# Kernel tuning notes

Hardware: AMD Instinct MI355X
Metric: run time of the kernel (lower is better)

Reference implementation:

```python
import jax, jax.numpy as jnp
import numpy as np
from functools import partial

U = 1200   # thought_size (GRU units)
E = 620    # word_size
V = 20000  # vocab_size
B = 128    # batch
T = 64     # seq_len
LN_EPS = 1e-3  # Keras LayerNormalization default epsilon


def layernorm(x, gamma, beta, eps=LN_EPS):
    m = jnp.mean(x, axis=-1, keepdims=True)
    v = jnp.mean(jnp.square(x - m), axis=-1, keepdims=True)
    return gamma * (x - m) * jax.lax.rsqrt(v + eps) + beta


def gru_ln_direction(emb, kernel, rkernel, bias, ln0_g, ln0_b, ln3_g, ln3_b):
    """Run the LayerNorm-GRU (impl=2, reset_after=True) over emb [B,T,E].
    Returns final hidden state [B,U]."""
    input_bias, recurrent_bias = bias[0], bias[1]
    # Time-parallel input projection: [B,T,3U]
    x_proj = jnp.einsum('bte,eu->btu', emb, kernel) + input_bias
    x_proj_t = jnp.transpose(x_proj, (1, 0, 2))  # [T,B,3U]

    def step(h, xt):
        h_ln = layernorm(h, ln0_g, ln0_b)                      # LN on previous state
        inner = h_ln @ rkernel + recurrent_bias                # [B,3U]
        z = jax.nn.sigmoid(xt[:, :U] + inner[:, :U])
        r = jax.nn.sigmoid(xt[:, U:2 * U] + inner[:, U:2 * U])
        rec_h = r * inner[:, 2 * U:]
        hh = jnp.tanh(layernorm(xt[:, 2 * U:] + rec_h, ln3_g, ln3_b))
        h_new = z * h_ln + (1.0 - z) * hh
        return h_new, None

    h0 = jnp.zeros((emb.shape[0], U), dtype=emb.dtype)
    h_final, _ = jax.lax.scan(step, h0, x_proj_t)
    return h_final


def setup_inputs() -> dict:
    key = jax.random.key(0)
    ks = jax.random.split(key, 8)
    s = 0.05
    return {
        'sentences': jax.random.randint(ks[0], (B, T), 0, V),
        'embed': jax.random.normal(ks[1], (V, E), jnp.float32) * s,
        'fw_kernel': jax.random.normal(ks[2], (E, 3 * U), jnp.float32) * s,
        'fw_rkernel': jax.random.normal(ks[3], (U, 3 * U), jnp.float32) * s,
        'fw_bias': jax.random.normal(ks[4], (2, 3 * U), jnp.float32) * s,
        'fw_ln0_g': jnp.ones((U,), jnp.float32),
        'fw_ln0_b': jnp.zeros((U,), jnp.float32),
        'fw_ln3_g': jnp.ones((U,), jnp.float32),
        'fw_ln3_b': jnp.zeros((U,), jnp.float32),
        'bw_kernel': jax.random.normal(ks[5], (E, 3 * U), jnp.float32) * s,
        'bw_rkernel': jax.random.normal(ks[6], (U, 3 * U), jnp.float32) * s,
        'bw_bias': jax.random.normal(ks[7], (2, 3 * U), jnp.float32) * s,
        'bw_ln0_g': jnp.ones((U,), jnp.float32),
        'bw_ln0_b': jnp.zeros((U,), jnp.float32),
        'bw_ln3_g': jnp.ones((U,), jnp.float32),
        'bw_ln3_b': jnp.zeros((U,), jnp.float32),
    }


def reference(sentences, embed, fw_kernel, fw_rkernel, fw_bias,
              fw_ln0_g, fw_ln0_b, fw_ln3_g, fw_ln3_b,
              bw_kernel, bw_rkernel, bw_bias,
              bw_ln0_g, bw_ln0_b, bw_ln3_g, bw_ln3_b):
    embedding = jnp.tanh(embed[sentences])  # [B,T,E]
    forward_h = gru_ln_direction(embedding, fw_kernel, fw_rkernel, fw_bias,
                                 fw_ln0_g, fw_ln0_b, fw_ln3_g, fw_ln3_b)
    backward_h = gru_ln_direction(embedding[:, ::-1, :], bw_kernel, bw_rkernel, bw_bias,
                                  bw_ln0_g, bw_ln0_b, bw_ln3_g, bw_ln3_b)
    thought_vector = jnp.concatenate([forward_h, backward_h], axis=1)  # [B,2U]
    return thought_vector, embedding
```

## Files before the change

kernel.cpp:

```cpp
#include <hip/hip_runtime.h>
#include <hip/hip_bf16.h>

#define U_    1200
#define E_    620
#define B_    128
#define T_    64
#define N3    3600
#define NP    3712
#define KE    640
#define KU    1216
#define WIN   16
#define LN_EPS 1e-3f

#define GBLK  464
#define UBLK  128
#define TBLK  (GBLK + UBLK)

typedef __attribute__((ext_vector_type(8))) short short8;
typedef __attribute__((ext_vector_type(4))) float f32x4;
typedef _Float16 f16;
typedef __attribute__((ext_vector_type(8))) _Float16 half8;

constexpr size_t OFF_EMBH  = 0;
constexpr size_t SZ_EMB    = (size_t)8192 * KE * 2;
constexpr size_t OFF_EMBL  = OFF_EMBH + SZ_EMB;
constexpr size_t OFF_KTH   = OFF_EMBL + SZ_EMB;
constexpr size_t SZ_KT     = (size_t)2 * NP * KE * 2;
constexpr size_t OFF_KTL   = OFF_KTH + SZ_KT;
constexpr size_t OFF_RKF   = OFF_KTL + SZ_KT;
constexpr size_t SZ_RKF    = (size_t)2 * NP * KU * 2;
constexpr size_t OFF_XPW   = OFF_RKF + SZ_RKF;
constexpr size_t SZ_XPW    = (size_t)2 * WIN * B_ * NP * 4;
constexpr size_t OFF_INNER = OFF_XPW + SZ_XPW;
constexpr size_t SZ_INNER  = (size_t)8 * B_ * NP * 4;
constexpr size_t OFF_HLN   = OFF_INNER + SZ_INNER;
constexpr size_t SZ_HLN    = (size_t)2 * B_ * U_ * 4;
constexpr size_t OFF_HLFH  = OFF_HLN + SZ_HLN;
constexpr size_t SZ_HLF    = (size_t)2 * B_ * KU * 2;
constexpr size_t OFF_HLFL  = OFF_HLFH + SZ_HLF;

__device__ inline void lds_load16(const void* g, void* l) {
  __builtin_amdgcn_global_load_lds(
      (const __attribute__((address_space(1))) unsigned int*)g,
      (__attribute__((address_space(3))) unsigned int*)l, 16, 0, 0);
}

__device__ inline float sigmf(float x) { return 1.f / (1.f + expf(-x)); }

__device__ inline int swz_scol(int tid) {
  return (((tid & 7) ^ ((tid >> 3) & 7)) << 3);
}
__device__ inline int swz_off(int row, int kk, int lane) {
  return row * 64 + ((kk * 32 + ((lane >> 4) << 3)) ^ ((row & 7) << 3));
}

__global__ __launch_bounds__(256)
void embed_kernel(const int* __restrict__ sent, const float* __restrict__ embed,
                  float* __restrict__ out_emb,
                  __hip_bfloat16* __restrict__ embH, __hip_bfloat16* __restrict__ embL) {
  const int row = blockIdx.x;
  const int idx = sent[row];
  const float* src = embed + (size_t)idx * E_;
  for (int e = threadIdx.x; e < KE; e += 256) {
    float v = 0.f;
    if (e < E_) {
      v = tanhf(src[e]);
      out_emb[(size_t)row * E_ + e] = v;
    }
    const __hip_bfloat16 hi = __float2bfloat16(v);
    embH[(size_t)row * KE + e] = hi;
    embL[(size_t)row * KE + e] = __float2bfloat16(v - __bfloat162float(hi));
  }
}

__global__ __launch_bounds__(256)
void transpose_cast(const float* __restrict__ W0, const float* __restrict__ W1,
                    __hip_bfloat16* __restrict__ WtHi, __hip_bfloat16* __restrict__ WtLo,
                    int Kreal, int Kp) {
  const int d = blockIdx.z;
  const float* W = d ? W1 : W0;
  __hip_bfloat16* dstH = WtHi + (size_t)d * NP * Kp;
  __hip_bfloat16* dstL = WtLo + (size_t)d * NP * Kp;
  __shared__ float tile[32][33];
  const int n0 = blockIdx.x * 32, k0 = blockIdx.y * 32;
  const int tx = threadIdx.x, ty = threadIdx.y;
#pragma unroll
  for (int i = 0; i < 32; i += 8) {
    const int k = k0 + ty + i, n = n0 + tx;
    tile[ty + i][tx] = (k < Kreal && n < N3) ? W[(size_t)k * N3 + n] : 0.f;
  }
  __syncthreads();
#pragma unroll
  for (int i = 0; i < 32; i += 8) {
    const int n = n0 + ty + i, k = k0 + tx;
    const float v = tile[tx][ty + i];
    const __hip_bfloat16 hi = __float2bfloat16(v);
    dstH[(size_t)n * Kp + k] = hi;
    dstL[(size_t)n * Kp + k] = __float2bfloat16(v - __bfloat162float(hi));
  }
}

__global__ __launch_bounds__(256)
void transpose_cast_f16(const float* __restrict__ W0, const float* __restrict__ W1,
                        f16* __restrict__ Wt, int Kreal, int Kp) {
  const int d = blockIdx.z;
  const float* W = d ? W1 : W0;
  f16* dst = Wt + (size_t)d * NP * Kp;
  __shared__ float tile[32][33];
  const int n0 = blockIdx.x * 32, k0 = blockIdx.y * 32;
  const int tx = threadIdx.x, ty = threadIdx.y;
#pragma unroll
  for (int i = 0; i < 32; i += 8) {
    const int k = k0 + ty + i, n = n0 + tx;
    tile[ty + i][tx] = (k < Kreal && n < N3) ? W[(size_t)k * N3 + n] : 0.f;
  }
  __syncthreads();
#pragma unroll
  for (int i = 0; i < 32; i += 8) {
    const int n = n0 + ty + i, k = k0 + tx;
    dst[(size_t)n * Kp + k] = (f16)tile[tx][ty + i];
  }
}

__global__ __launch_bounds__(256)
void init_hln(const float* __restrict__ fw_b0, const float* __restrict__ bw_b0,
              float* __restrict__ hln, f16* __restrict__ hlfH, f16* __restrict__ hlfL) {
  const int idx = blockIdx.x * 256 + threadIdx.x;
  if (idx >= 2 * B_ * KU) return;
  const int k = idx % KU;
  const int rowd = idx / KU;
  const int d = rowd >> 7;
  float v = 0.f;
  if (k < U_) {
    v = (d ? bw_b0 : fw_b0)[k];
    hln[(size_t)rowd * U_ + k] = v;
  }
  const f16 hi = (f16)v;
  hlfH[idx] = hi;
  hlfL[idx] = (f16)(v - (float)hi);
}

__global__ __launch_bounds__(256)
void xwin_gemm(const __hip_bfloat16* __restrict__ embH, const __hip_bfloat16* __restrict__ embL,
               const __hip_bfloat16* __restrict__ kTH, const __hip_bfloat16* __restrict__ kTL,
               const float* __restrict__ fw_bias, const float* __restrict__ bw_bias,
               float* __restrict__ xpw, int w0) {
  constexpr int BM = 128, BN = 128, BK = 64;
  constexpr int WM = 64, WN = 64, FM = 4, FN = 4;
  constexpr int TA = BM * BK, TB = BN * BK;
  const int bid = blockIdx.x;
  const int w = (bid & 7) * 116 + (bid >> 3);
  const int d = w / 464;
  const int q = w % 464;
  const int nt = q / 16, mt = q % 16;
  const int m0 = mt * BM;
  const int n0 = nt * BN;

  const __hip_bfloat16* BH = kTH + (size_t)d * NP * KE;
  const __hip_bfloat16* BL = kTL + (size_t)d * NP * KE;

  const int tid = threadIdx.x;
  const int lane = tid & 63;
  const int wid = tid >> 6;
  const int wr = wid >> 1, wc = wid & 1;

  __shared__ __align__(16) __hip_bfloat16 As[2 * TA];
  __shared__ __align__(16) __hip_bfloat16 Bs[2 * TB];

  f32x4 acc[FM][FN] = {};

  const int srow = tid >> 3;
  const int scol = swz_scol(tid);

  for (int ks = 0; ks < KE / BK; ++ks) {
    const int k0 = ks * BK;
    __syncthreads();
#pragma unroll
    for (int it = 0; it < TA / 2048; ++it) {
      const int row = m0 + it * 32 + srow;
      const int b = row & 127, srel = row >> 7;
      const int txi = d ? (T_ - 1 - (w0 + srel)) : (w0 + srel);
      const size_t goff = (size_t)(b * T_ + txi) * KE + k0 + scol;
      lds_load16(embH + goff, As + it * 2048 + tid * 8);
      lds_load16(embL + goff, As + TA + it * 2048 + tid * 8);
    }
#pragma unroll
    for (int it = 0; it < TB / 2048; ++it) {
      const size_t goff = (size_t)(n0 + it * 32 + srow) * KE + k0 + scol;
      lds_load16(BH + goff, Bs + it * 2048 + tid * 8);
      lds_load16(BL + goff, Bs + TB + it * 2048 + tid * 8);
    }
    __syncthreads();
#pragma unroll
    for (int kk = 0; kk < BK / 32; ++kk) {
      short8 ah[FM], al[FM], bh[FN], bl[FN];
#pragma unroll
      for (int mi = 0; mi < FM; ++mi) {
        const int row = wr * WM + mi * 16 + (lane & 15);
        const int off = swz_off(row, kk, lane);
        ah[mi] = *(const short8*)(As + off);
        al[mi] = *(const short8*)(As + TA + off);
      }
#pragma unroll
      for (int ni = 0; ni < FN; ++ni) {
        const int row = wc * WN + ni * 16 + (lane & 15);
        const int off = swz_off(row, kk, lane);
        bh[ni] = *(const short8*)(Bs + off);
        bl[ni] = *(const short8*)(Bs + TB + off);
      }
#pragma unroll
      for (int mi = 0; mi < FM; ++mi)
#pragma unroll
        for (int ni = 0; ni < FN; ++ni) {
          acc[mi][ni] = __builtin_amdgcn_mfma_f32_16x16x32_bf16(ah[mi], bh[ni], acc[mi][ni], 0, 0, 0);
          acc[mi][ni] = __builtin_amdgcn_mfma_f32_16x16x32_bf16(ah[mi], bl[ni], acc[mi][ni], 0, 0, 0);
          acc[mi][ni] = __builtin_amdgcn_mfma_f32_16x16x32_bf16(al[mi], bh[ni], acc[mi][ni], 0, 0, 0);
        }
    }
  }

  const float* ib = d ? bw_bias : fw_bias;
#pragma unroll
  for (int mi = 0; mi < FM; ++mi)
#pragma unroll
    for (int ni = 0; ni < FN; ++ni) {
      const int gc = n0 + wc * WN + ni * 16 + (lane & 15);
      const float bv = (gc < N3) ? ib[gc] : 0.f;
      const int gr0 = m0 + wr * WM + mi * 16 + ((lane >> 4) << 2);
#pragma unroll
      for (int j = 0; j < 4; ++j) {
        const int gr = gr0 + j;
        const int b = gr & 127, srel = gr >> 7;
        const size_t off = ((size_t)(d * WIN + srel) * B_ + b) * NP + gc;
        xpw[off] = acc[mi][ni][j] + bv;
      }
    }
}

__device__ inline void breduce2(float& a, float& b, float* red, int tid) {
#pragma unroll
  for (int off = 32; off; off >>= 1) {
    a += __shfl_down(a, off, 64);
    b += __shfl_down(b, off, 64);
  }
  const int w = tid >> 6;
  __syncthreads();
  if ((tid & 63) == 0) { red[w] = a; red[4 + w] = b; }
  __syncthreads();
  a = red[0] + red[1] + red[2] + red[3];
  b = red[4] + red[5] + red[6] + red[7];
}

__global__ __launch_bounds__(256)
void step_fused(const f16* __restrict__ rkF,
                f16* __restrict__ hlfH, f16* __restrict__ hlfL,
                float* __restrict__ hln, float* __restrict__ inner,
                const float* __restrict__ xpw,
                const float* __restrict__ fw_bias, const float* __restrict__ bw_bias,
                const float* __restrict__ fw_ln0g, const float* __restrict__ fw_ln0b,
                const float* __restrict__ fw_ln3g, const float* __restrict__ fw_ln3b,
                const float* __restrict__ bw_ln0g, const float* __restrict__ bw_ln0b,
                const float* __restrict__ bw_ln3g, const float* __restrict__ bw_ln3b,
                float* __restrict__ out_tv,
                int dG, int doG, int dU, int tU, int doU) {
  __shared__ __align__(16) f16 smem[24576];
  __shared__ float red[8];

  const int bid = blockIdx.x;
  const int tid = threadIdx.x;

  if (bid < GBLK) {
    if (!doG) return;
    const int x  = bid & 7;
    const int kp = x >> 1;
    const int m  = x & 1;
    const int nt = bid >> 3;
    const int ks0 = kp * 5;
    const int ks1 = (kp == 3) ? 19 : (ks0 + 5);
    const int m0 = m * 64;
    const int n0 = nt * 64;

    const int lane = tid & 63;
    const int wid = tid >> 6;
    const int wr = wid >> 1, wc = wid & 1;

    const f16* WF = rkF + (size_t)dG * NP * KU;

    f32x4 acc[2][2] = {};
    const int srow = tid >> 3;
    const int scol = swz_scol(tid);

#define STG(buf_, ks_)                                                         \
  {                                                                            \
    const int k0s = (ks_) * 64;                                                \
    f16* base = smem + (buf_) * 12288;                                         \
    _Pragma("unroll")                                                          \
    for (int it = 0; it < 2; ++it) {                                           \
      const size_t ga = (size_t)(dG * B_ + m0 + it * 32 + srow) * KU + k0s + scol; \
      lds_load16(hlfH + ga, base + it * 2048 + tid * 8);                       \
      lds_load16(hlfL + ga, base + 4096 + it * 2048 + tid * 8);                \
      const size_t gb = (size_t)(n0 + it * 32 + srow) * KU + k0s + scol;       \
      lds_load16(WF + gb, base + 8192 + it * 2048 + tid * 8);                  \
    }                                                                          \
  }

    STG(0, ks0)
    __syncthreads();
    int cur = 0;
    for (int ks = ks0; ks < ks1; ++ks) {
      if (ks + 1 < ks1) STG(cur ^ 1, ks + 1)
      const f16* AH = smem + cur * 12288;
      const f16* AL = AH + 4096;
      const f16* BW = AH + 8192;
#pragma unroll
      for (int kk = 0; kk < 2; ++kk) {
        half8 ah[2], al[2], bv[2];
#pragma unroll
        for (int mi = 0; mi < 2; ++mi) {
          const int row = wr * 32 + mi * 16 + (lane & 15);
          const int off = swz_off(row, kk, lane);
          ah[mi] = *(const half8*)(AH + off);
          al[mi] = *(const half8*)(AL + off);
        }
#pragma unroll
        for (int nf = 0; nf < 2; ++nf) {
          const int row = wc * 32 + nf * 16 + (lane & 15);
          const int off = swz_off(row, kk, lane);
          bv[nf] = *(const half8*)(BW + off);
        }
#pragma unroll
        for (int mi = 0; mi < 2; ++mi)
#pragma unroll
          for (int nf = 0; nf < 2; ++nf) {
            acc[mi][nf] = __builtin_amdgcn_mfma_f32_16x16x32_f16(ah[mi], bv[nf], acc[mi][nf], 0, 0, 0);
            acc[mi][nf] = __builtin_amdgcn_mfma_f32_16x16x32_f16(al[mi], bv[nf], acc[mi][nf], 0, 0, 0);
          }
      }
      __syncthreads();
      cur ^= 1;
    }
#undef STG

    float* C = inner + (size_t)(dG * 4 + kp) * B_ * NP;
#pragma unroll
    for (int mi = 0; mi < 2; ++mi)
#pragma unroll
      for (int nf = 0; nf < 2; ++nf) {
        const int gc = n0 + wc * 32 + nf * 16 + (lane & 15);
        const int gr = m0 + wr * 32 + mi * 16 + ((lane >> 4) << 2);
#pragma unroll
        for (int j = 0; j < 4; ++j)
          C[(size_t)(gr + j) * NP + gc] = acc[mi][nf][j];
      }
    return;
  }

  if (!doU) return;
  const int r = bid - GBLK;
  const int d = dU;
  const int srel = tU & (WIN - 1);

  const float* rec0 = inner + ((size_t)(d * 4 + 0) * B_ + r) * NP;
  const float* rec1 = inner + ((size_t)(d * 4 + 1) * B_ + r) * NP;
  const float* rec2 = inner + ((size_t)(d * 4 + 2) * B_ + r) * NP;
  const float* rec3 = inner + ((size_t)(d * 4 + 3) * B_ + r) * NP;
  const float* xr = xpw + ((size_t)(d * WIN + srel) * B_ + r) * NP;
  const float* rb = (d ? bw_bias : fw_bias) + N3;
  const float* g0 = d ? bw_ln0g : fw_ln0g;
  const float* b0 = d ? bw_ln0b : fw_ln0b;
  const float* g3 = d ? bw_ln3g : fw_ln3g;
  const float* b3 = d ? bw_ln3b : fw_ln3b;
  float* hl = hln + ((size_t)d * B_ + r) * U_;
  f16* hlbH = hlfH + ((size_t)d * B_ + r) * KU;
  f16* hlbL = hlfL + ((size_t)d * B_ + r) * KU;

  float zv[5], cv[5], hv[5];
  float s1 = 0.f, s2 = 0.f;
#pragma unroll
  for (int i = 0; i < 5; ++i) {
    const int c = tid + i * 256;
    if (c < U_) {
      const float rz = (rec0[c] + rec1[c]) + (rec2[c] + rec3[c]);
      const float rg = (rec0[U_ + c] + rec1[U_ + c]) + (rec2[U_ + c] + rec3[U_ + c]);
      const float rh = (rec0[2 * U_ + c] + rec1[2 * U_ + c]) + (rec2[2 * U_ + c] + rec3[2 * U_ + c]);
      const float z  = sigmf(xr[c] + rz + rb[c]);
      const float rr = sigmf(xr[U_ + c] + rg + rb[U_ + c]);
      const float cand = xr[2 * U_ + c] + rr * (rh + rb[2 * U_ + c]);
      zv[i] = z; cv[i] = cand;
      s1 += cand; s2 += cand * cand;
    }
  }
  breduce2(s1, s2, red, tid);
  const float m1 = s1 / U_;
  const float is1 = rsqrtf(s2 / U_ - m1 * m1 + LN_EPS);

  float t1 = 0.f, t2 = 0.f;
#pragma unroll
  for (int i = 0; i < 5; ++i) {
    const int c = tid + i * 256;
    if (c < U_) {
      const float hh = tanhf(g3[c] * (cv[i] - m1) * is1 + b3[c]);
      const float hn = zv[i] * hl[c] + (1.f - zv[i]) * hh;
      hv[i] = hn;
      t1 += hn; t2 += hn * hn;
    }
  }
  breduce2(t1, t2, red, tid);
  const float m2 = t1 / U_;
  const float is2 = rsqrtf(t2 / U_ - m2 * m2 + LN_EPS);

#pragma unroll
  for (int i = 0; i < 5; ++i) {
    const int c = tid + i * 256;
    if (c < U_) {
      const float hlnew = g0[c] * (hv[i] - m2) * is2 + b0[c];
      hl[c] = hlnew;
      const f16 hi = (f16)hlnew;
      hlbH[c] = hi;
      hlbL[c] = (f16)(hlnew - (float)hi);
      if (tU == T_ - 1) out_tv[(size_t)r * 2400 + (size_t)d * U_ + c] = hv[i];
    }
  }
}

extern "C" void kernel_launch(void* const* d_in, const int* in_sizes, int n_in,
                              void* d_out, int out_size, void* d_ws, size_t ws_size,
                              hipStream_t stream) {
  const int*   sent      = (const int*)  d_in[0];
  const float* embed     = (const float*)d_in[1];
  const float* fw_kernel = (const float*)d_in[2];
  const float* fw_rkern  = (const float*)d_in[3];
  const float* fw_bias   = (const float*)d_in[4];
  const float* fw_ln0g   = (const float*)d_in[5];
  const float* fw_ln0b   = (const float*)d_in[6];
  const float* fw_ln3g   = (const float*)d_in[7];
  const float* fw_ln3b   = (const float*)d_in[8];
  const float* bw_kernel = (const float*)d_in[9];
  const float* bw_rkern  = (const float*)d_in[10];
  const float* bw_bias   = (const float*)d_in[11];
  const float* bw_ln0g   = (const float*)d_in[12];
  const float* bw_ln0b   = (const float*)d_in[13];
  const float* bw_ln3g   = (const float*)d_in[14];
  const float* bw_ln3b   = (const float*)d_in[15];

  uint8_t* ws = (uint8_t*)d_ws;
  __hip_bfloat16* embH  = (__hip_bfloat16*)(ws + OFF_EMBH);
  __hip_bfloat16* embL  = (__hip_bfloat16*)(ws + OFF_EMBL);
  __hip_bfloat16* kTH   = (__hip_bfloat16*)(ws + OFF_KTH);
  __hip_bfloat16* kTL   = (__hip_bfloat16*)(ws + OFF_KTL);
  f16*            rkF   = (f16*)(ws + OFF_RKF);
  float*          xpw   = (float*)(ws + OFF_XPW);
  float*          inner = (float*)(ws + OFF_INNER);
  float*          hln   = (float*)(ws + OFF_HLN);
  f16*            hlfH  = (f16*)(ws + OFF_HLFH);
  f16*            hlfL  = (f16*)(ws + OFF_HLFL);

  float* out_tv  = (float*)d_out;
  float* out_emb = (float*)d_out + (size_t)B_ * 2 * U_;

  embed_kernel<<<B_ * T_, 256, 0, stream>>>(sent, embed, out_emb, embH, embL);

  transpose_cast<<<dim3(NP / 32, KE / 32, 2), dim3(32, 8), 0, stream>>>(
      fw_kernel, bw_kernel, kTH, kTL, E_, KE);
  transpose_cast_f16<<<dim3(NP / 32, KU / 32, 2), dim3(32, 8), 0, stream>>>(
      fw_rkern, bw_rkern, rkF, U_, KU);

  init_hln<<<(2 * B_ * KU + 255) / 256, 256, 0, stream>>>(fw_ln0b, bw_ln0b,
                                                          hln, hlfH, hlfL);

#define SF(dG_, doG_, dU_, tU_, doU_)                                          \
  step_fused<<<TBLK, 256, 0, stream>>>(                                        \
      rkF, hlfH, hlfL, hln, inner, xpw,                                        \
      fw_bias, bw_bias, fw_ln0g, fw_ln0b, fw_ln3g, fw_ln3b,                    \
      bw_ln0g, bw_ln0b, bw_ln3g, bw_ln3b, out_tv,                              \
      dG_, doG_, dU_, tU_, doU_)

  for (int t = 0; t < T_; ++t) {
    SF(0, 1, 1, t - 1, (t > 0) ? 1 : 0);
    if ((t & (WIN - 1)) == 0)
      xwin_gemm<<<928, 256, 0, stream>>>(
          embH, embL, kTH, kTL, fw_bias, bw_bias, xpw, t);
    SF(1, 1, 0, t, 1);
  }
  SF(0, 0, 1, T_ - 1, 1);
#undef SF
}
```

Baseline: 1.788 ms.

## Fuse GRU step GEMM and update into one launch with flag-based sync

Before, each timestep ran as two staggered launches that interleaved one direction's GEMM with the other direction's update. Now one launch per timestep runs both directions' recurrent GEMM blocks and 256 update blocks. Update blocks spin on atomic counters in global memory until all GEMM blocks for their direction have stored their partial results. This halves the number of launches and removes the cross-direction stagger. The risk is a deadlock or stall if update blocks occupy CUs before the GEMM blocks get scheduled, plus the cost of relaxed atomic loads and stores on the partial results.

```diff
diff --git a/kernel.cpp b/kernel.cpp
--- a/kernel.cpp
+++ b/kernel.cpp
@@ -13,8 +13,7 @@
 #define LN_EPS 1e-3f
 
 #define GBLK  464
-#define UBLK  128
-#define TBLK  (GBLK + UBLK)
+#define TBLK  (2 * GBLK + 256)
 
 typedef __attribute__((ext_vector_type(8))) short short8;
 typedef __attribute__((ext_vector_type(4))) float f32x4;
@@ -38,6 +37,7 @@
 constexpr size_t OFF_HLFH  = OFF_HLN + SZ_HLN;
 constexpr size_t SZ_HLF    = (size_t)2 * B_ * KU * 2;
 constexpr size_t OFF_HLFL  = OFF_HLFH + SZ_HLF;
+constexpr size_t OFF_FLAGS = OFF_HLFL + SZ_HLF;
 
 __device__ inline void lds_load16(const void* g, void* l) {
   __builtin_amdgcn_global_load_lds(
@@ -46,6 +46,13 @@
 }
 
 __device__ inline float sigmf(float x) { return 1.f / (1.f + expf(-x)); }
+
+__device__ inline void astore(float* p, float v) {
+  __hip_atomic_store(p, v, __ATOMIC_RELAXED, __HIP_MEMORY_SCOPE_AGENT);
+}
+__device__ inline float aload(const float* p) {
+  return __hip_atomic_load(p, __ATOMIC_RELAXED, __HIP_MEMORY_SCOPE_AGENT);
+}
 
 __device__ inline int swz_scol(int tid) {
   return (((tid & 7) ^ ((tid >> 3) & 7)) << 3);
@@ -252,29 +259,29 @@
 }
 
 __global__ __launch_bounds__(256)
-void step_fused(const f16* __restrict__ rkF,
-                f16* __restrict__ hlfH, f16* __restrict__ hlfL,
-                float* __restrict__ hln, float* __restrict__ inner,
-                const float* __restrict__ xpw,
-                const float* __restrict__ fw_bias, const float* __restrict__ bw_bias,
-                const float* __restrict__ fw_ln0g, const float* __restrict__ fw_ln0b,
-                const float* __restrict__ fw_ln3g, const float* __restrict__ fw_ln3b,
-                const float* __restrict__ bw_ln0g, const float* __restrict__ bw_ln0b,
-                const float* __restrict__ bw_ln3g, const float* __restrict__ bw_ln3b,
-                float* __restrict__ out_tv,
-                int dG, int doG, int dU, int tU, int doU) {
+void step_all(const f16* __restrict__ rkF,
+              f16* __restrict__ hlfH, f16* __restrict__ hlfL,
+              float* __restrict__ hln, float* __restrict__ inner,
+              const float* __restrict__ xpw, int* __restrict__ flags,
+              const float* __restrict__ fw_bias, const float* __restrict__ bw_bias,
+              const float* __restrict__ fw_ln0g, const float* __restrict__ fw_ln0b,
+              const float* __restrict__ fw_ln3g, const float* __restrict__ fw_ln3b,
+              const float* __restrict__ bw_ln0g, const float* __restrict__ bw_ln0b,
+              const float* __restrict__ bw_ln3g, const float* __restrict__ bw_ln3b,
+              float* __restrict__ out_tv, int t) {
   __shared__ __align__(16) f16 smem[24576];
   __shared__ float red[8];
 
   const int bid = blockIdx.x;
   const int tid = threadIdx.x;
 
-  if (bid < GBLK) {
-    if (!doG) return;
-    const int x  = bid & 7;
+  if (bid < 2 * GBLK) {
+    const int dG = bid >= GBLK;
+    const int b2 = bid - dG * GBLK;
+    const int x  = b2 & 7;
     const int kp = x >> 1;
     const int m  = x & 1;
-    const int nt = bid >> 3;
+    const int nt = b2 >> 3;
     const int ks0 = kp * 5;
     const int ks1 = (kp == 3) ? 19 : (ks0 + 5);
     const int m0 = m * 64;
@@ -350,15 +357,26 @@
         const int gr = m0 + wr * 32 + mi * 16 + ((lane >> 4) << 2);
 #pragma unroll
         for (int j = 0; j < 4; ++j)
-          C[(size_t)(gr + j) * NP + gc] = acc[mi][nf][j];
+          astore(&C[(size_t)(gr + j) * NP + gc], acc[mi][nf][j]);
       }
+    __syncthreads();
+    if (tid == 0)
+      __hip_atomic_fetch_add(&flags[2 * t + dG], 1, __ATOMIC_RELAXED,
+                             __HIP_MEMORY_SCOPE_AGENT);
     return;
   }
 
-  if (!doU) return;
-  const int r = bid - GBLK;
-  const int d = dU;
-  const int srel = tU & (WIN - 1);
+  const int u = bid - 2 * GBLK;
+  const int d = u >> 7;
+  const int r = u & 127;
+  const int srel = t & (WIN - 1);
+
+  if (tid == 0) {
+    while (__hip_atomic_load(&flags[2 * t + d], __ATOMIC_RELAXED,
+                             __HIP_MEMORY_SCOPE_AGENT) < GBLK)
+      __builtin_amdgcn_s_sleep(8);
+  }
+  __syncthreads();
 
   const float* rec0 = inner + ((size_t)(d * 4 + 0) * B_ + r) * NP;
   const float* rec1 = inner + ((size_t)(d * 4 + 1) * B_ + r) * NP;
@@ -380,9 +398,12 @@
   for (int i = 0; i < 5; ++i) {
     const int c = tid + i * 256;
     if (c < U_) {
-      const float rz = (rec0[c] + rec1[c]) + (rec2[c] + rec3[c]);
-      const float rg = (rec0[U_ + c] + rec1[U_ + c]) + (rec2[U_ + c] + rec3[U_ + c]);
-      const float rh = (rec0[2 * U_ + c] + rec1[2 * U_ + c]) + (rec2[2 * U_ + c] + rec3[2 * U_ + c]);
+      const float rz = (aload(&rec0[c]) + aload(&rec1[c])) +
+                       (aload(&rec2[c]) + aload(&rec3[c]));
+      const float rg = (aload(&rec0[U_ + c]) + aload(&rec1[U_ + c])) +
+                       (aload(&rec2[U_ + c]) + aload(&rec3[U_ + c]));
+      const float rh = (aload(&rec0[2 * U_ + c]) + aload(&rec1[2 * U_ + c])) +
+                       (aload(&rec2[2 * U_ + c]) + aload(&rec3[2 * U_ + c]));
       const float z  = sigmf(xr[c] + rz + rb[c]);
       const float rr = sigmf(xr[U_ + c] + rg + rb[U_ + c]);
       const float cand = xr[2 * U_ + c] + rr * (rh + rb[2 * U_ + c]);
@@ -418,7 +439,7 @@
       const f16 hi = (f16)hlnew;
       hlbH[c] = hi;
       hlbL[c] = (f16)(hlnew - (float)hi);
-      if (tU == T_ - 1) out_tv[(size_t)r * 2400 + (size_t)d * U_ + c] = hv[i];
+      if (t == T_ - 1) out_tv[(size_t)r * 2400 + (size_t)d * U_ + c] = hv[i];
     }
   }
 }
@@ -454,9 +475,12 @@
   float*          hln   = (float*)(ws + OFF_HLN);
   f16*            hlfH  = (f16*)(ws + OFF_HLFH);
   f16*            hlfL  = (f16*)(ws + OFF_HLFL);
+  int*            flags = (int*)(ws + OFF_FLAGS);
 
   float* out_tv  = (float*)d_out;
   float* out_emb = (float*)d_out + (size_t)B_ * 2 * U_;
+
+  hipMemsetAsync(flags, 0, 2 * T_ * sizeof(int), stream);
 
   embed_kernel<<<B_ * T_, 256, 0, stream>>>(sent, embed, out_emb, embH, embL);
 
@@ -468,20 +492,13 @@
   init_hln<<<(2 * B_ * KU + 255) / 256, 256, 0, stream>>>(fw_ln0b, bw_ln0b,
                                                           hln, hlfH, hlfL);
 
-#define SF(dG_, doG_, dU_, tU_, doU_)                                          \
-  step_fused<<<TBLK, 256, 0, stream>>>(                                        \
-      rkF, hlfH, hlfL, hln, inner, xpw,                                        \
-      fw_bias, bw_bias, fw_ln0g, fw_ln0b, fw_ln3g, fw_ln3b,                    \
-      bw_ln0g, bw_ln0b, bw_ln3g, bw_ln3b, out_tv,                              \
-      dG_, doG_, dU_, tU_, doU_)
-
   for (int t = 0; t < T_; ++t) {
-    SF(0, 1, 1, t - 1, (t > 0) ? 1 : 0);
     if ((t & (WIN - 1)) == 0)
       xwin_gemm<<<928, 256, 0, stream>>>(
           embH, embL, kTH, kTL, fw_bias, bw_bias, xpw, t);
-    SF(1, 1, 0, t, 1);
-  }
-  SF(0, 0, 1, T_ - 1, 1);
-#undef SF
-}
+    step_all<<<TBLK, 256, 0, stream>>>(
+        rkF, hlfH, hlfL, hln, inner, xpw, flags,
+        fw_bias, bw_bias, fw_ln0g, fw_ln0b, fw_ln3g, fw_ln3b,
+        bw_ln0g, bw_ln0b, bw_ln3g, bw_ln3b, out_tv, t);
+  }
+}
```

Measured after the change: 3.123 ms. 1.75x slower.

## Fuse both GRU directions into one launch per step with in-kernel flag sync

Applied to the files above, without the earlier changes.

Each timestep previously took two launches, each pairing one direction's recurrent GEMM with the other direction's gate update. Now a single launch per step runs the gate-update blocks for both directions alongside GEMM blocks for both directions. The GEMM blocks spin on per-step atomic counters until all 128 update rows of their direction have written the new hidden state. Split-K drops from 4 to 2, the inner partials become parity double-buffered, and the LDS double buffering in the GEMM loop is removed. This roughly halves launch count and per-launch sync overhead. In exchange it depends on update blocks being scheduled before the spinning GEMM blocks, relies on relaxed atomics without explicit fences for visibility, and loses load/compute overlap in the GEMM.

```diff
diff --git a/kernel.cpp b/kernel.cpp
--- a/kernel.cpp
+++ b/kernel.cpp
@@ -12,9 +12,9 @@
 #define WIN   16
 #define LN_EPS 1e-3f
 
+#define UBLK  256
 #define GBLK  464
-#define UBLK  128
-#define TBLK  (GBLK + UBLK)
+#define TBLK  (UBLK + GBLK)
 
 typedef __attribute__((ext_vector_type(8))) short short8;
 typedef __attribute__((ext_vector_type(4))) float f32x4;
@@ -38,6 +38,7 @@
 constexpr size_t OFF_HLFH  = OFF_HLN + SZ_HLN;
 constexpr size_t SZ_HLF    = (size_t)2 * B_ * KU * 2;
 constexpr size_t OFF_HLFL  = OFF_HLFH + SZ_HLF;
+constexpr size_t OFF_FLAGS = OFF_HLFL + SZ_HLF;
 
 __device__ inline void lds_load16(const void* g, void* l) {
   __builtin_amdgcn_global_load_lds(
@@ -46,6 +47,10 @@
 }
 
 __device__ inline float sigmf(float x) { return 1.f / (1.f + expf(-x)); }
+
+__device__ inline void astore_u16(unsigned short* p, unsigned short v) {
+  __hip_atomic_store(p, v, __ATOMIC_RELAXED, __HIP_MEMORY_SCOPE_AGENT);
+}
 
 __device__ inline int swz_scol(int tid) {
   return (((tid & 7) ^ ((tid >> 3) & 7)) << 3);
@@ -252,33 +257,44 @@
 }
 
 __global__ __launch_bounds__(256)
-void step_fused(const f16* __restrict__ rkF,
-                f16* __restrict__ hlfH, f16* __restrict__ hlfL,
-                float* __restrict__ hln, float* __restrict__ inner,
-                const float* __restrict__ xpw,
-                const float* __restrict__ fw_bias, const float* __restrict__ bw_bias,
-                const float* __restrict__ fw_ln0g, const float* __restrict__ fw_ln0b,
-                const float* __restrict__ fw_ln3g, const float* __restrict__ fw_ln3b,
-                const float* __restrict__ bw_ln0g, const float* __restrict__ bw_ln0b,
-                const float* __restrict__ bw_ln3g, const float* __restrict__ bw_ln3b,
-                float* __restrict__ out_tv,
-                int dG, int doG, int dU, int tU, int doU) {
-  __shared__ __align__(16) f16 smem[24576];
+void step_one(const f16* __restrict__ rkF,
+              f16* __restrict__ hlfH, f16* __restrict__ hlfL,
+              float* __restrict__ hln, float* __restrict__ inner,
+              const float* __restrict__ xpw, int* __restrict__ flags,
+              const float* __restrict__ fw_bias, const float* __restrict__ bw_bias,
+              const float* __restrict__ fw_ln0g, const float* __restrict__ fw_ln0b,
+              const float* __restrict__ fw_ln3g, const float* __restrict__ fw_ln3b,
+              const float* __restrict__ bw_ln0g, const float* __restrict__ bw_ln0b,
+              const float* __restrict__ bw_ln3g, const float* __restrict__ bw_ln3b,
+              float* __restrict__ out_tv, int t, int doU, int doG) {
+  __shared__ __align__(16) f16 smem[12288];
   __shared__ float red[8];
 
   const int bid = blockIdx.x;
   const int tid = threadIdx.x;
 
-  if (bid < GBLK) {
+  if (bid >= UBLK) {
     if (!doG) return;
-    const int x  = bid & 7;
+    const int bid2 = bid - UBLK;
+    const int dG = bid2 >= 232;
+    const int b2 = bid2 - dG * 232;
+    const int x  = b2 & 3;
     const int kp = x >> 1;
     const int m  = x & 1;
-    const int nt = bid >> 3;
-    const int ks0 = kp * 5;
-    const int ks1 = (kp == 3) ? 19 : (ks0 + 5);
+    const int nt = b2 >> 2;
+    const int ks0 = kp ? 10 : 0;
+    const int ks1 = kp ? 19 : 10;
     const int m0 = m * 64;
     const int n0 = nt * 64;
+
+    if (doU) {
+      if (tid == 0) {
+        while (__hip_atomic_load(&flags[2 * t + dG], __ATOMIC_RELAXED,
+                                 __HIP_MEMORY_SCOPE_AGENT) < B_)
+          __builtin_amdgcn_s_sleep(2);
+      }
+      __syncthreads();
+    }
 
     const int lane = tid & 63;
     const int wid = tid >> 6;
@@ -290,28 +306,18 @@
     const int srow = tid >> 3;
     const int scol = swz_scol(tid);
 
-#define STG(buf_, ks_)                                                         \
-  {                                                                            \
-    const int k0s = (ks_) * 64;                                                \
-    f16* base = smem + (buf_) * 12288;                                         \
-    _Pragma("unroll")                                                          \
-    for (int it = 0; it < 2; ++it) {                                           \
-      const size_t ga = (size_t)(dG * B_ + m0 + it * 32 + srow) * KU + k0s + scol; \
-      lds_load16(hlfH + ga, base + it * 2048 + tid * 8);                       \
-      lds_load16(hlfL + ga, base + 4096 + it * 2048 + tid * 8);                \
-      const size_t gb = (size_t)(n0 + it * 32 + srow) * KU + k0s + scol;       \
-      lds_load16(WF + gb, base + 8192 + it * 2048 + tid * 8);                  \
-    }                                                                          \
-  }
-
-    STG(0, ks0)
-    __syncthreads();
-    int cur = 0;
     for (int ks = ks0; ks < ks1; ++ks) {
-      if (ks + 1 < ks1) STG(cur ^ 1, ks + 1)
-      const f16* AH = smem + cur * 12288;
-      const f16* AL = AH + 4096;
-      const f16* BW = AH + 8192;
+      const int k0s = ks * 64;
+      __syncthreads();
+#pragma unroll
+      for (int it = 0; it < 2; ++it) {
+        const size_t ga = (size_t)(dG * B_ + m0 + it * 32 + srow) * KU + k0s + scol;
+        lds_load16(hlfH + ga, smem + it * 2048 + tid * 8);
+        lds_load16(hlfL + ga, smem + 4096 + it * 2048 + tid * 8);
+        const size_t gb = (size_t)(n0 + it * 32 + srow) * KU + k0s + scol;
+        lds_load16(WF + gb, smem + 8192 + it * 2048 + tid * 8);
+      }
+      __syncthreads();
 #pragma unroll
       for (int kk = 0; kk < 2; ++kk) {
         half8 ah[2], al[2], bv[2];
@@ -319,14 +325,14 @@
         for (int mi = 0; mi < 2; ++mi) {
           const int row = wr * 32 + mi * 16 + (lane & 15);
           const int off = swz_off(row, kk, lane);
-          ah[mi] = *(const half8*)(AH + off);
-          al[mi] = *(const half8*)(AL + off);
+          ah[mi] = *(const half8*)(smem + off);
+          al[mi] = *(const half8*)(smem + 4096 + off);
         }
 #pragma unroll
         for (int nf = 0; nf < 2; ++nf) {
           const int row = wc * 32 + nf * 16 + (lane & 15);
           const int off = swz_off(row, kk, lane);
-          bv[nf] = *(const half8*)(BW + off);
+          bv[nf] = *(const half8*)(smem + 8192 + off);
         }
 #pragma unroll
         for (int mi = 0; mi < 2; ++mi)
@@ -336,12 +342,9 @@
             acc[mi][nf] = __builtin_amdgcn_mfma_f32_16x16x32_f16(al[mi], bv[nf], acc[mi][nf], 0, 0, 0);
           }
       }
-      __syncthreads();
-      cur ^= 1;
-    }
-#undef STG
-
-    float* C = inner + (size_t)(dG * 4 + kp) * B_ * NP;
+    }
+
+    float* C = inner + (size_t)((t & 1) * 4 + dG * 2 + kp) * B_ * NP;
 #pragma unroll
     for (int mi = 0; mi < 2; ++mi)
 #pragma unroll
@@ -356,14 +359,13 @@
   }
 
   if (!doU) return;
-  const int r = bid - GBLK;
-  const int d = dU;
+  const int tU = t - 1;
+  const int d = bid >> 7;
+  const int r = bid & 127;
   const int srel = tU & (WIN - 1);
 
-  const float* rec0 = inner + ((size_t)(d * 4 + 0) * B_ + r) * NP;
-  const float* rec1 = inner + ((size_t)(d * 4 + 1) * B_ + r) * NP;
-  const float* rec2 = inner + ((size_t)(d * 4 + 2) * B_ + r) * NP;
-  const float* rec3 = inner + ((size_t)(d * 4 + 3) * B_ + r) * NP;
+  const float* rec0 = inner + ((size_t)((tU & 1) * 4 + d * 2 + 0) * B_ + r) * NP;
+  const float* rec1 = inner + ((size_t)((tU & 1) * 4 + d * 2 + 1) * B_ + r) * NP;
   const float* xr = xpw + ((size_t)(d * WIN + srel) * B_ + r) * NP;
   const float* rb = (d ? bw_bias : fw_bias) + N3;
   const float* g0 = d ? bw_ln0g : fw_ln0g;
@@ -380,9 +382,9 @@
   for (int i = 0; i < 5; ++i) {
     const int c = tid + i * 256;
     if (c < U_) {
-      const float rz = (rec0[c] + rec1[c]) + (rec2[c] + rec3[c]);
-      const float rg = (rec0[U_ + c] + rec1[U_ + c]) + (rec2[U_ + c] + rec3[U_ + c]);
-      const float rh = (rec0[2 * U_ + c] + rec1[2 * U_ + c]) + (rec2[2 * U_ + c] + rec3[2 * U_ + c]);
+      const float rz = rec0[c] + rec1[c];
+      const float rg = rec0[U_ + c] + rec1[U_ + c];
+      const float rh = rec0[2 * U_ + c] + rec1[2 * U_ + c];
       const float z  = sigmf(xr[c] + rz + rb[c]);
       const float rr = sigmf(xr[U_ + c] + rg + rb[U_ + c]);
       const float cand = xr[2 * U_ + c] + rr * (rh + rb[2 * U_ + c]);
@@ -416,11 +418,16 @@
       const float hlnew = g0[c] * (hv[i] - m2) * is2 + b0[c];
       hl[c] = hlnew;
       const f16 hi = (f16)hlnew;
-      hlbH[c] = hi;
-      hlbL[c] = (f16)(hlnew - (float)hi);
+      const f16 lo = (f16)(hlnew - (float)hi);
+      astore_u16((unsigned short*)&hlbH[c], __builtin_bit_cast(unsigned short, hi));
+      astore_u16((unsigned short*)&hlbL[c], __builtin_bit_cast(unsigned short, lo));
       if (tU == T_ - 1) out_tv[(size_t)r * 2400 + (size_t)d * U_ + c] = hv[i];
     }
   }
+  __syncthreads();
+  if (tid == 0)
+    __hip_atomic_fetch_add(&flags[2 * t + d], 1, __ATOMIC_RELAXED,
+                           __HIP_MEMORY_SCOPE_AGENT);
 }
 
 extern "C" void kernel_launch(void* const* d_in, const int* in_sizes, int n_in,
@@ -454,9 +461,12 @@
   float*          hln   = (float*)(ws + OFF_HLN);
   f16*            hlfH  = (f16*)(ws + OFF_HLFH);
   f16*            hlfL  = (f16*)(ws + OFF_HLFL);
+  int*            flags = (int*)(ws + OFF_FLAGS);
 
   float* out_tv  = (float*)d_out;
   float* out_emb = (float*)d_out + (size_t)B_ * 2 * U_;
+
+  hipMemsetAsync(flags, 0, 2 * (T_ + 1) * sizeof(int), stream);
 
   embed_kernel<<<B_ * T_, 256, 0, stream>>>(sent, embed, out_emb, embH, embL);
 
@@ -468,20 +478,18 @@
   init_hln<<<(2 * B_ * KU + 255) / 256, 256, 0, stream>>>(fw_ln0b, bw_ln0b,
                                                           hln, hlfH, hlfL);
 
-#define SF(dG_, doG_, dU_, tU_, doU_)                                          \
-  step_fused<<<TBLK, 256, 0, stream>>>(                                        \
-      rkF, hlfH, hlfL, hln, inner, xpw,                                        \
+#define SO(t_, doU_, doG_)                                                     \
+  step_one<<<TBLK, 256, 0, stream>>>(                                          \
+      rkF, hlfH, hlfL, hln, inner, xpw, flags,                                 \
       fw_bias, bw_bias, fw_ln0g, fw_ln0b, fw_ln3g, fw_ln3b,                    \
-      bw_ln0g, bw_ln0b, bw_ln3g, bw_ln3b, out_tv,                              \
-      dG_, doG_, dU_, tU_, doU_)
+      bw_ln0g, bw_ln0b, bw_ln3g, bw_ln3b, out_tv, t_, doU_, doG_)
 
   for (int t = 0; t < T_; ++t) {
-    SF(0, 1, 1, t - 1, (t > 0) ? 1 : 0);
+    SO(t, (t > 0) ? 1 : 0, 1);
     if ((t & (WIN - 1)) == 0)
       xwin_gemm<<<928, 256, 0, stream>>>(
           embH, embL, kTH, kTL, fw_bias, bw_bias, xpw, t);
-    SF(1, 1, 0, t, 1);
-  }
-  SF(0, 0, 1, T_ - 1, 1);
-#undef SF
-}
+  }
+  SO(T_, 1, 0);
+#undef SO
+}
```

After: 2.179 ms. 1.22x slower.

## Overlap next-window input projection GEMM with recurrent step kernels

Applied to the files above, without the earlier changes.

Removes the separate xwin_gemm launch every 16 steps. The next window's input projection is now spread across 120 extra blocks in each fused step launch, writing into a double-buffered xpw. Those blocks run the bf16 hi/lo split GEMM while the recurrent GEMM and update blocks run, so otherwise idle CUs get work and the periodic serial GEMM stall goes away. In exchange the workspace grows, the launch grid gets larger, and the step kernel uses more LDS (48KB static), which may lower occupancy.

```diff
diff --git a/kernel.cpp b/kernel.cpp
--- a/kernel.cpp
+++ b/kernel.cpp
@@ -14,7 +14,9 @@
 
 #define GBLK  464
 #define UBLK  128
-#define TBLK  (GBLK + UBLK)
+#define XBLK  120
+#define TBLK  (GBLK + UBLK + XBLK)
+#define XJOBS 3712
 
 typedef __attribute__((ext_vector_type(8))) short short8;
 typedef __attribute__((ext_vector_type(4))) float f32x4;
@@ -30,7 +32,8 @@
 constexpr size_t OFF_RKF   = OFF_KTL + SZ_KT;
 constexpr size_t SZ_RKF    = (size_t)2 * NP * KU * 2;
 constexpr size_t OFF_XPW   = OFF_RKF + SZ_RKF;
-constexpr size_t SZ_XPW    = (size_t)2 * WIN * B_ * NP * 4;
+constexpr size_t SZ_XPW1   = (size_t)2 * WIN * B_ * NP * 4;
+constexpr size_t SZ_XPW    = 2 * SZ_XPW1;
 constexpr size_t OFF_INNER = OFF_XPW + SZ_XPW;
 constexpr size_t SZ_INNER  = (size_t)8 * B_ * NP * 4;
 constexpr size_t OFF_HLN   = OFF_INNER + SZ_INNER;
@@ -255,15 +258,17 @@
 void step_fused(const f16* __restrict__ rkF,
                 f16* __restrict__ hlfH, f16* __restrict__ hlfL,
                 float* __restrict__ hln, float* __restrict__ inner,
-                const float* __restrict__ xpw,
+                float* __restrict__ xpw,
+                const __hip_bfloat16* __restrict__ embH, const __hip_bfloat16* __restrict__ embL,
+                const __hip_bfloat16* __restrict__ kTH, const __hip_bfloat16* __restrict__ kTL,
                 const float* __restrict__ fw_bias, const float* __restrict__ bw_bias,
                 const float* __restrict__ fw_ln0g, const float* __restrict__ fw_ln0b,
                 const float* __restrict__ fw_ln3g, const float* __restrict__ fw_ln3b,
                 const float* __restrict__ bw_ln0g, const float* __restrict__ bw_ln0b,
                 const float* __restrict__ bw_ln3g, const float* __restrict__ bw_ln3b,
                 float* __restrict__ out_tv,
-                int dG, int doG, int dU, int tU, int doU) {
-  __shared__ __align__(16) f16 smem[24576];
+                int dG, int doG, int dU, int tU, int doU, int xw, int xjob0) {
+  __shared__ __align__(16) unsigned char sraw[49152];
   __shared__ float red[8];
 
   const int bid = blockIdx.x;
@@ -285,6 +290,7 @@
     const int wr = wid >> 1, wc = wid & 1;
 
     const f16* WF = rkF + (size_t)dG * NP * KU;
+    f16* smem = (f16*)sraw;
 
     f32x4 acc[2][2] = {};
     const int srow = tid >> 3;
@@ -355,72 +361,163 @@
     return;
   }
 
-  if (!doU) return;
-  const int r = bid - GBLK;
-  const int d = dU;
-  const int srel = tU & (WIN - 1);
-
-  const float* rec0 = inner + ((size_t)(d * 4 + 0) * B_ + r) * NP;
-  const float* rec1 = inner + ((size_t)(d * 4 + 1) * B_ + r) * NP;
-  const float* rec2 = inner + ((size_t)(d * 4 + 2) * B_ + r) * NP;
-  const float* rec3 = inner + ((size_t)(d * 4 + 3) * B_ + r) * NP;
-  const float* xr = xpw + ((size_t)(d * WIN + srel) * B_ + r) * NP;
-  const float* rb = (d ? bw_bias : fw_bias) + N3;
-  const float* g0 = d ? bw_ln0g : fw_ln0g;
-  const float* b0 = d ? bw_ln0b : fw_ln0b;
-  const float* g3 = d ? bw_ln3g : fw_ln3g;
-  const float* b3 = d ? bw_ln3b : fw_ln3b;
-  float* hl = hln + ((size_t)d * B_ + r) * U_;
-  f16* hlbH = hlfH + ((size_t)d * B_ + r) * KU;
-  f16* hlbL = hlfL + ((size_t)d * B_ + r) * KU;
-
-  float zv[5], cv[5], hv[5];
-  float s1 = 0.f, s2 = 0.f;
-#pragma unroll
-  for (int i = 0; i < 5; ++i) {
-    const int c = tid + i * 256;
-    if (c < U_) {
-      const float rz = (rec0[c] + rec1[c]) + (rec2[c] + rec3[c]);
-      const float rg = (rec0[U_ + c] + rec1[U_ + c]) + (rec2[U_ + c] + rec3[U_ + c]);
-      const float rh = (rec0[2 * U_ + c] + rec1[2 * U_ + c]) + (rec2[2 * U_ + c] + rec3[2 * U_ + c]);
-      const float z  = sigmf(xr[c] + rz + rb[c]);
-      const float rr = sigmf(xr[U_ + c] + rg + rb[U_ + c]);
-      const float cand = xr[2 * U_ + c] + rr * (rh + rb[2 * U_ + c]);
-      zv[i] = z; cv[i] = cand;
-      s1 += cand; s2 += cand * cand;
-    }
-  }
-  breduce2(s1, s2, red, tid);
-  const float m1 = s1 / U_;
-  const float is1 = rsqrtf(s2 / U_ - m1 * m1 + LN_EPS);
-
-  float t1 = 0.f, t2 = 0.f;
-#pragma unroll
-  for (int i = 0; i < 5; ++i) {
-    const int c = tid + i * 256;
-    if (c < U_) {
-      const float hh = tanhf(g3[c] * (cv[i] - m1) * is1 + b3[c]);
-      const float hn = zv[i] * hl[c] + (1.f - zv[i]) * hh;
-      hv[i] = hn;
-      t1 += hn; t2 += hn * hn;
-    }
-  }
-  breduce2(t1, t2, red, tid);
-  const float m2 = t1 / U_;
-  const float is2 = rsqrtf(t2 / U_ - m2 * m2 + LN_EPS);
-
-#pragma unroll
-  for (int i = 0; i < 5; ++i) {
-    const int c = tid + i * 256;
-    if (c < U_) {
-      const float hlnew = g0[c] * (hv[i] - m2) * is2 + b0[c];
-      hl[c] = hlnew;
-      const f16 hi = (f16)hlnew;
-      hlbH[c] = hi;
-      hlbL[c] = (f16)(hlnew - (float)hi);
-      if (tU == T_ - 1) out_tv[(size_t)r * 2400 + (size_t)d * U_ + c] = hv[i];
-    }
-  }
+  if (bid < GBLK + UBLK) {
+    if (!doU) return;
+    const int r = bid - GBLK;
+    const int d = dU;
+    const int srel = tU & (WIN - 1);
+    const int ubuf = (tU >> 4) & 1;
+
+    const float* rec0 = inner + ((size_t)(d * 4 + 0) * B_ + r) * NP;
+    const float* rec1 = inner + ((size_t)(d * 4 + 1) * B_ + r) * NP;
+    const float* rec2 = inner + ((size_t)(d * 4 + 2) * B_ + r) * NP;
+    const float* rec3 = inner + ((size_t)(d * 4 + 3) * B_ + r) * NP;
+    const float* xr = xpw + (size_t)ubuf * (2 * WIN * B_ * NP) +
+                      ((size_t)(d * WIN + srel) * B_ + r) * NP;
+    const float* rb = (d ? bw_bias : fw_bias) + N3;
+    const float* g0 = d ? bw_ln0g : fw_ln0g;
+    const float* b0 = d ? bw_ln0b : fw_ln0b;
+    const float* g3 = d ? bw_ln3g : fw_ln3g;
+    const float* b3 = d ? bw_ln3b : fw_ln3b;
+    float* hl = hln + ((size_t)d * B_ + r) * U_;
+    f16* hlbH = hlfH + ((size_t)d * B_ + r) * KU;
+    f16* hlbL = hlfL + ((size_t)d * B_ + r) * KU;
+
+    float zv[5], cv[5], hv[5];
+    float s1 = 0.f, s2 = 0.f;
+#pragma unroll
+    for (int i = 0; i < 5; ++i) {
+      const int c = tid + i * 256;
+      if (c < U_) {
+        const float rz = (rec0[c] + rec1[c]) + (rec2[c] + rec3[c]);
+        const float rg = (rec0[U_ + c] + rec1[U_ + c]) + (rec2[U_ + c] + rec3[U_ + c]);
+        const float rh = (rec0[2 * U_ + c] + rec1[2 * U_ + c]) + (rec2[2 * U_ + c] + rec3[2 * U_ + c]);
+        const float z  = sigmf(xr[c] + rz + rb[c]);
+        const float rr = sigmf(xr[U_ + c] + rg + rb[U_ + c]);
+        const float cand = xr[2 * U_ + c] + rr * (rh + rb[2 * U_ + c]);
+        zv[i] = z; cv[i] = cand;
+        s1 += cand; s2 += cand * cand;
+      }
+    }
+    breduce2(s1, s2, red, tid);
+    const float m1 = s1 / U_;
+    const float is1 = rsqrtf(s2 / U_ - m1 * m1 + LN_EPS);
+
+    float t1 = 0.f, t2 = 0.f;
+#pragma unroll
+    for (int i = 0; i < 5; ++i) {
+      const int c = tid + i * 256;
+      if (c < U_) {
+        const float hh = tanhf(g3[c] * (cv[i] - m1) * is1 + b3[c]);
+        const float hn = zv[i] * hl[c] + (1.f - zv[i]) * hh;
+        hv[i] = hn;
+        t1 += hn; t2 += hn * hn;
+      }
+    }
+    breduce2(t1, t2, red, tid);
+    const float m2 = t1 / U_;
+    const float is2 = rsqrtf(t2 / U_ - m2 * m2 + LN_EPS);
+
+#pragma unroll
+    for (int i = 0; i < 5; ++i) {
+      const int c = tid + i * 256;
+      if (c < U_) {
+        const float hlnew = g0[c] * (hv[i] - m2) * is2 + b0[c];
+        hl[c] = hlnew;
+        const f16 hi = (f16)hlnew;
+        hlbH[c] = hi;
+        hlbL[c] = (f16)(hlnew - (float)hi);
+        if (tU == T_ - 1) out_tv[(size_t)r * 2400 + (size_t)d * U_ + c] = hv[i];
+      }
+    }
+    return;
+  }
+
+  if (xw < 0) return;
+  const int j = xjob0 + (bid - GBLK - UBLK);
+  if (j >= XJOBS) return;
+  const int d = j / (XJOBS / 2);
+  const int rem = j % (XJOBS / 2);
+  const int nt = rem / 32, mt = rem % 32;
+  const int m0 = mt * 64;
+  const int n0 = nt * 64;
+  float* xp = xpw + (size_t)(xw & 1) * (2 * WIN * B_ * NP);
+
+  const __hip_bfloat16* BH = kTH + (size_t)d * NP * KE;
+  const __hip_bfloat16* BL = kTL + (size_t)d * NP * KE;
+
+  const int lane = tid & 63;
+  const int wid = tid >> 6;
+  const int wr = wid >> 1, wc = wid & 1;
+
+  __hip_bfloat16* AsH = (__hip_bfloat16*)sraw;
+  __hip_bfloat16* AsL = AsH + 4096;
+  __hip_bfloat16* BsH = AsH + 8192;
+  __hip_bfloat16* BsL = AsH + 12288;
+
+  f32x4 acc[2][2] = {};
+  const int srow = tid >> 3;
+  const int scol = swz_scol(tid);
+
+  for (int ks = 0; ks < KE / 64; ++ks) {
+    const int k0 = ks * 64;
+    __syncthreads();
+#pragma unroll
+    for (int it = 0; it < 2; ++it) {
+      const int row = m0 + it * 32 + srow;
+      const int b = row & 127, srel = row >> 7;
+      const int txi = d ? (T_ - 1 - (xw * WIN + srel)) : (xw * WIN + srel);
+      const size_t ga = (size_t)(b * T_ + txi) * KE + k0 + scol;
+      lds_load16(embH + ga, AsH + it * 2048 + tid * 8);
+      lds_load16(embL + ga, AsL + it * 2048 + tid * 8);
+      const size_t gb = (size_t)(n0 + it * 32 + srow) * KE + k0 + scol;
+      lds_load16(BH + gb, BsH + it * 2048 + tid * 8);
+      lds_load16(BL + gb, BsL + it * 2048 + tid * 8);
+    }
+    __syncthreads();
+#pragma unroll
+    for (int kk = 0; kk < 2; ++kk) {
+      short8 ah[2], al[2], bh[2], bl[2];
+#pragma unroll
+      for (int mi = 0; mi < 2; ++mi) {
+        const int row = wr * 32 + mi * 16 + (lane & 15);
+        const int off = swz_off(row, kk, lane);
+        ah[mi] = *(const short8*)(AsH + off);
+        al[mi] = *(const short8*)(AsL + off);
+      }
+#pragma unroll
+      for (int nf = 0; nf < 2; ++nf) {
+        const int row = wc * 32 + nf * 16 + (lane & 15);
+        const int off = swz_off(row, kk, lane);
+        bh[nf] = *(const short8*)(BsH + off);
+        bl[nf] = *(const short8*)(BsL + off);
+      }
+#pragma unroll
+      for (int mi = 0; mi < 2; ++mi)
+#pragma unroll
+        for (int nf = 0; nf < 2; ++nf) {
+          acc[mi][nf] = __builtin_amdgcn_mfma_f32_16x16x32_bf16(ah[mi], bh[nf], acc[mi][nf], 0, 0, 0);
+          acc[mi][nf] = __builtin_amdgcn_mfma_f32_16x16x32_bf16(ah[mi], bl[nf], acc[mi][nf], 0, 0, 0);
+          acc[mi][nf] = __builtin_amdgcn_mfma_f32_16x16x32_bf16(al[mi], bh[nf], acc[mi][nf], 0, 0, 0);
+        }
+    }
+  }
+
+  const float* ib = d ? bw_bias : fw_bias;
+#pragma unroll
+  for (int mi = 0; mi < 2; ++mi)
+#pragma unroll
+    for (int nf = 0; nf < 2; ++nf) {
+      const int gc = n0 + wc * 32 + nf * 16 + (lane & 15);
+      const float bv = (gc < N3) ? ib[gc] : 0.f;
+      const int gr0 = m0 + wr * 32 + mi * 16 + ((lane >> 4) << 2);
+#pragma unroll
+      for (int jj = 0; jj < 4; ++jj) {
+        const int gr = gr0 + jj;
+        const int b = gr & 127, srel = gr >> 7;
+        xp[((size_t)(d * WIN + srel) * B_ + b) * NP + gc] = acc[mi][nf][jj] + bv;
+      }
+    }
 }
 
 extern "C" void kernel_launch(void* const* d_in, const int* in_sizes, int n_in,
@@ -468,20 +565,27 @@
   init_hln<<<(2 * B_ * KU + 255) / 256, 256, 0, stream>>>(fw_ln0b, bw_ln0b,
                                                           hln, hlfH, hlfL);
 
-#define SF(dG_, doG_, dU_, tU_, doU_)                                          \
+  xwin_gemm<<<928, 256, 0, stream>>>(
+      embH, embL, kTH, kTL, fw_bias, bw_bias, xpw, 0);
+
+#define SF(dG_, doG_, dU_, tU_, doU_, xw_, xj_)                                \
   step_fused<<<TBLK, 256, 0, stream>>>(                                        \
-      rkF, hlfH, hlfL, hln, inner, xpw,                                        \
+      rkF, hlfH, hlfL, hln, inner, xpw, embH, embL, kTH, kTL,                  \
       fw_bias, bw_bias, fw_ln0g, fw_ln0b, fw_ln3g, fw_ln3b,                    \
       bw_ln0g, bw_ln0b, bw_ln3g, bw_ln3b, out_tv,                              \
-      dG_, doG_, dU_, tU_, doU_)
+      dG_, doG_, dU_, tU_, doU_, xw_, xj_)
 
   for (int t = 0; t < T_; ++t) {
-    SF(0, 1, 1, t - 1, (t > 0) ? 1 : 0);
-    if ((t & (WIN - 1)) == 0)
-      xwin_gemm<<<928, 256, 0, stream>>>(
-          embH, embL, kTH, kTL, fw_bias, bw_bias, xpw, t);
-    SF(1, 1, 0, t, 1);
-  }
-  SF(0, 0, 1, T_ - 1, 1);
+    const int w = t >> 4;
+    const int kord0 = 2 * (t & (WIN - 1));
+    int xwA = -1, xjA = 0, xwB = -1, xjB = 0;
+    if (w < 3) {
+      if (kord0 >= 1)     { xwA = w + 1; xjA = (kord0 - 1) * XBLK; }
+      if (kord0 + 1 >= 1) { xwB = w + 1; xjB = (kord0 + 0) * XBLK; }
+    }
+    SF(0, 1, 1, t - 1, (t > 0) ? 1 : 0, xwA, xjA);
+    SF(1, 1, 0, t, 1, xwB, xjB);
+  }
+  SF(0, 0, 1, T_ - 1, 1, -1, 0);
 #undef SF
 }
```

Result: slower. 1.879 ms (+5.0%).
